# Optimization experiments

Hardware: AMD Instinct MI355X
Metric: run time of the kernel (lower is better)

Reference implementation:

```python
import jax, jax.numpy as jnp
import numpy as np

N = 131072   # number of profile points
S = 64       # n_samples (PSF samples per point)
D = H = W = 256


def setup_inputs() -> dict:
    key = jax.random.key(0)
    k1, k2, k3, k4, k5, k6 = jax.random.split(key, 6)
    x = jax.random.normal(k1, (1, 1, D, H, W), dtype=jnp.float32)
    # voxel-space coordinates (x, y, z) inside the volume
    sampleGrid = jax.random.uniform(k2, (N, 3), dtype=jnp.float32) * jnp.array(
        [W - 1, H - 1, D - 1], dtype=jnp.float32)
    # small axis-angle rotations + translations: [N, 1, 6]
    rot = jax.random.normal(k3, (N, 1, 3), dtype=jnp.float32) * 0.02
    trn = jax.random.normal(k4, (N, 1, 3), dtype=jnp.float32) * 2.0
    ax = jnp.concatenate([rot, trn], axis=-1)
    half = jax.random.uniform(k5, (N, 1, 3), minval=1.0, maxval=3.0, dtype=jnp.float32)
    bound = jnp.concatenate([-half, half], axis=1)  # [N, 2, 3]
    InvCovScaled = jnp.eye(3, dtype=jnp.float32) * 0.5
    # torch.randn(...) - 0.5 from the original forward, hoisted out for determinism
    xyz_psf = jax.random.normal(k6, (N, S, 3), dtype=jnp.float32) - 0.5
    return dict(x=x, sampleGrid=sampleGrid, ax=ax, bound=bound,
                InvCovScaled=InvCovScaled, xyz_psf=xyz_psf)


def _axisangle2mat(a):
    # a: [N, 6] -> [N, 3, 4] = [R | t] via Rodrigues
    v, t = a[:, :3], a[:, 3:]
    theta = jnp.linalg.norm(v, axis=-1, keepdims=True)          # [N,1]
    k = v / jnp.maximum(theta, 1e-12)                            # unit axis
    kx, ky, kz = k[:, 0], k[:, 1], k[:, 2]
    z = jnp.zeros_like(kx)
    K = jnp.stack([z, -kz, ky, kz, z, -kx, -ky, kx, z], axis=-1).reshape(-1, 3, 3)
    ct = jnp.cos(theta)[..., None]  # [N,1,1]
    st = jnp.sin(theta)[..., None]
    I = jnp.eye(3, dtype=a.dtype)
    R = I + st * K + (1.0 - ct) * jnp.matmul(K, K)
    return jnp.concatenate([R, t[..., None]], axis=-1)           # [N,3,4]


def _grid_sample_3d(vol, grid):
    # vol: [D,H,W]; grid: [M,3] normalized coords (x,y,z) in [-1,1]
    # matches F.grid_sample(mode='bilinear', padding_mode='zeros', align_corners=False)
    d, h, w = vol.shape
    sizes = jnp.array([w, h, d], dtype=vol.dtype)
    pix = ((grid + 1.0) * sizes - 1.0) * 0.5                     # unnormalize
    ix, iy, iz = pix[:, 0], pix[:, 1], pix[:, 2]
    x0 = jnp.floor(ix); y0 = jnp.floor(iy); z0 = jnp.floor(iz)
    fx = ix - x0; fy = iy - y0; fz = iz - z0
    x0 = x0.astype(jnp.int32); y0 = y0.astype(jnp.int32); z0 = z0.astype(jnp.int32)

    def gather(xi, yi, zi):
        valid = ((xi >= 0) & (xi < w) & (yi >= 0) & (yi < h) & (zi >= 0) & (zi < d))
        xc = jnp.clip(xi, 0, w - 1)
        yc = jnp.clip(yi, 0, h - 1)
        zc = jnp.clip(zi, 0, d - 1)
        return jnp.where(valid, vol[zc, yc, xc], jnp.zeros((), vol.dtype))

    out = jnp.zeros(grid.shape[0], dtype=vol.dtype)
    for dx in (0, 1):
        wx = fx if dx else (1.0 - fx)
        for dy in (0, 1):
            wy = fy if dy else (1.0 - fy)
            for dz in (0, 1):
                wz = fz if dz else (1.0 - fz)
                out = out + gather(x0 + dx, y0 + dy, z0 + dz) * (wx * wy * wz)
    return out


def reference(x, sampleGrid, ax, bound, InvCovScaled, xyz_psf):
    vol = x[0, 0]                                                # [D,H,W]
    size = jnp.array([x.shape[-1], x.shape[-2], x.shape[-3]], dtype=x.dtype)  # [W,H,D]

    # pose matrices [N,1,3,4]
    mat = _axisangle2mat(ax.reshape(-1, 6)).reshape(ax.shape[:-1] + (3, 4))
    R = mat[..., :3]                                             # [N,1,3,3]
    T = mat[..., 3]                                              # [N,1,3]
    # trans_first=True: p' = R @ (p + T)
    p = sampleGrid[:, None] + T                                  # [N,1,3]
    mat_sampleGrid = jnp.einsum('nkij,nkj->nki', R, p)           # [N,1,3]

    # PSF offsets: [N,S,3]
    bound_psf = xyz_psf * ((bound[:, 1, :] - bound[:, 0, :]) * 0.5)[:, None]
    psf = mat_sampleGrid + bound_psf                             # [N,S,3]

    grid = 2.0 * (psf / (size - 1.0) - 0.5)                      # normalize per-axis
    psf_x = _grid_sample_3d(vol, grid.reshape(-1, 3)).reshape(psf.shape[:-1])  # [N,S]

    center = bound_psf
    q = jnp.einsum('nsi,ij,nsj->ns', center, InvCovScaled, center)
    w = jnp.exp(-0.5 * q)                                        # [N,S]
    y = (psf_x * w).sum(-1) / w.sum(-1)                          # [N]
    return y
```

## Files before the change

kernel.cpp:

```cpp
#include <hip/hip_runtime.h>


#define VOL_N 256
#define S_PSF 64

__global__ __launch_bounds__(256, 4) void psf_sample_kernel(
    const float* __restrict__ vol,
    const float* __restrict__ sampleGrid,
    const float* __restrict__ ax,
    const float* __restrict__ bound,
    const float* __restrict__ invcov,
    const float* __restrict__ xyz_psf,
    float* __restrict__ out,
    int N)
{
    const int lane = threadIdx.x & 63;
    const int n = blockIdx.x * (blockDim.x >> 6) + (threadIdx.x >> 6);
    if (n >= N) return;

    const float vx = ax[n * 6 + 0], vy = ax[n * 6 + 1], vz = ax[n * 6 + 2];
    const float tx = ax[n * 6 + 3], ty = ax[n * 6 + 4], tz = ax[n * 6 + 5];

    const float theta = sqrtf(vx * vx + vy * vy + vz * vz);
    const float kinv = 1.0f / fmaxf(theta, 1e-12f);
    const float kx = vx * kinv, ky = vy * kinv, kz = vz * kinv;
    const float ct = __cosf(theta), st = __sinf(theta);
    const float oc = 1.0f - ct;

    const float r00 = 1.0f + oc * (-(ky * ky + kz * kz));
    const float r01 = -st * kz + oc * kx * ky;
    const float r02 =  st * ky + oc * kx * kz;
    const float r10 =  st * kz + oc * kx * ky;
    const float r11 = 1.0f + oc * (-(kx * kx + kz * kz));
    const float r12 = -st * kx + oc * ky * kz;
    const float r20 = -st * ky + oc * kx * kz;
    const float r21 =  st * kx + oc * ky * kz;
    const float r22 = 1.0f + oc * (-(kx * kx + ky * ky));

    const float px = sampleGrid[n * 3 + 0] + tx;
    const float py = sampleGrid[n * 3 + 1] + ty;
    const float pz = sampleGrid[n * 3 + 2] + tz;

    const float cx = r00 * px + r01 * py + r02 * pz;
    const float cy = r10 * px + r11 * py + r12 * pz;
    const float cz = r20 * px + r21 * py + r22 * pz;

    const float hx = (bound[n * 6 + 3] - bound[n * 6 + 0]) * 0.5f;
    const float hy = (bound[n * 6 + 4] - bound[n * 6 + 1]) * 0.5f;
    const float hz = (bound[n * 6 + 5] - bound[n * 6 + 2]) * 0.5f;

    const float m00 = invcov[0], m01 = invcov[1], m02 = invcov[2];
    const float m10 = invcov[3], m11 = invcov[4], m12 = invcov[5];
    const float m20 = invcov[6], m21 = invcov[7], m22 = invcov[8];

    const long long base = ((long long)n * S_PSF + lane) * 3;
    const float ox = xyz_psf[base + 0] * hx;
    const float oy = xyz_psf[base + 1] * hy;
    const float oz = xyz_psf[base + 2] * hz;

    const float scale = (float)VOL_N / (float)(VOL_N - 1);
    const float ix = (cx + ox) * scale - 0.5f;
    const float iy = (cy + oy) * scale - 0.5f;
    const float iz = (cz + oz) * scale - 0.5f;

    const float x0f = floorf(ix), y0f = floorf(iy), z0f = floorf(iz);
    const float fx = ix - x0f, fy = iy - y0f, fz = iz - z0f;
    const int x0 = (int)x0f, y0 = (int)y0f, z0 = (int)z0f;
    const int x1 = x0 + 1, y1 = y0 + 1, z1 = z0 + 1;

    const bool vx0 = (unsigned)x0 < (unsigned)VOL_N;
    const bool vx1 = (unsigned)x1 < (unsigned)VOL_N;
    const bool vy0 = (unsigned)y0 < (unsigned)VOL_N;
    const bool vy1 = (unsigned)y1 < (unsigned)VOL_N;
    const bool vz0 = (unsigned)z0 < (unsigned)VOL_N;
    const bool vz1 = (unsigned)z1 < (unsigned)VOL_N;

    const int xc0 = min(max(x0, 0), VOL_N - 1);
    const int xc1 = min(max(x1, 0), VOL_N - 1);
    const int yc0 = min(max(y0, 0), VOL_N - 1);
    const int yc1 = min(max(y1, 0), VOL_N - 1);
    const int zc0 = min(max(z0, 0), VOL_N - 1);
    const int zc1 = min(max(z1, 0), VOL_N - 1);

    const int zo0 = zc0 * (VOL_N * VOL_N), zo1 = zc1 * (VOL_N * VOL_N);
    const int yo0 = yc0 * VOL_N, yo1 = yc1 * VOL_N;

    const float v000 = vol[zo0 + yo0 + xc0];
    const float v001 = vol[zo0 + yo0 + xc1];
    const float v010 = vol[zo0 + yo1 + xc0];
    const float v011 = vol[zo0 + yo1 + xc1];
    const float v100 = vol[zo1 + yo0 + xc0];
    const float v101 = vol[zo1 + yo0 + xc1];
    const float v110 = vol[zo1 + yo1 + xc0];
    const float v111 = vol[zo1 + yo1 + xc1];

    const float wx0 = 1.0f - fx, wx1 = fx;
    const float wy0 = 1.0f - fy, wy1 = fy;
    const float wz0 = 1.0f - fz, wz1 = fz;

    float acc = 0.0f;
    acc += (vx0 && vy0 && vz0) ? v000 * (wx0 * wy0 * wz0) : 0.0f;
    acc += (vx1 && vy0 && vz0) ? v001 * (wx1 * wy0 * wz0) : 0.0f;
    acc += (vx0 && vy1 && vz0) ? v010 * (wx0 * wy1 * wz0) : 0.0f;
    acc += (vx1 && vy1 && vz0) ? v011 * (wx1 * wy1 * wz0) : 0.0f;
    acc += (vx0 && vy0 && vz1) ? v100 * (wx0 * wy0 * wz1) : 0.0f;
    acc += (vx1 && vy0 && vz1) ? v101 * (wx1 * wy0 * wz1) : 0.0f;
    acc += (vx0 && vy1 && vz1) ? v110 * (wx0 * wy1 * wz1) : 0.0f;
    acc += (vx1 && vy1 && vz1) ? v111 * (wx1 * wy1 * wz1) : 0.0f;

    const float qx = m00 * ox + m01 * oy + m02 * oz;
    const float qy = m10 * ox + m11 * oy + m12 * oz;
    const float qz = m20 * ox + m21 * oy + m22 * oz;
    const float q = ox * qx + oy * qy + oz * qz;
    const float w = __expf(-0.5f * q);

    float num = acc * w;
    float den = w;
    #pragma unroll
    for (int m = 32; m >= 1; m >>= 1) {
        num += __shfl_xor(num, m, 64);
        den += __shfl_xor(den, m, 64);
    }
    if (lane == 0) out[n] = num / den;
}

extern "C" void kernel_launch(void* const* d_in, const int* in_sizes, int n_in,
                              void* d_out, int out_size, void* d_ws, size_t ws_size,
                              hipStream_t stream) {
    const float* x        = (const float*)d_in[0];
    const float* sg       = (const float*)d_in[1];
    const float* ax       = (const float*)d_in[2];
    const float* bound    = (const float*)d_in[3];
    const float* invcov   = (const float*)d_in[4];
    const float* xyz_psf  = (const float*)d_in[5];
    float* out            = (float*)d_out;

    const int N = in_sizes[1] / 3;
    const int waves_per_block = 4;
    dim3 block(256);
    dim3 grid((N + waves_per_block - 1) / waves_per_block);
    psf_sample_kernel<<<grid, block, 0, stream>>>(x, sg, ax, bound, invcov,
                                                  xyz_psf, out, N);
}
```

Measured before the change: 337.8 us.

## Sort profile points by Morton-ordered spatial bucket to improve volume cache locality

Adds histogram, scan and scatter kernels that bucket the N points by the Morton code of their coarse 16-voxel cell, producing a permutation used by the main kernel. The main kernel also remaps block IDs across the eight XCDs so contiguous sorted chunks share each XCD's L2. The goal is to turn random 64MB volume gathers into spatially coherent accesses with better L2/MALL hit rates. In exchange it adds four small kernel launches, global atomics, and an indirection that makes reads of ax, bound, xyz_psf and out non-coalesced.

```diff
diff --git a/kernel.cpp b/kernel.cpp
--- a/kernel.cpp
+++ b/kernel.cpp
@@ -3,6 +3,61 @@
 
 #define VOL_N 256
 #define S_PSF 64
+#define NBUCKET 4096
+
+
+__device__ __forceinline__ int bucket_of(const float* __restrict__ sg, int n) {
+    int cx = min(max((int)sg[n * 3 + 0], 0), VOL_N - 1) >> 4;
+    int cy = min(max((int)sg[n * 3 + 1], 0), VOL_N - 1) >> 4;
+    int cz = min(max((int)sg[n * 3 + 2], 0), VOL_N - 1) >> 4;
+    int m = 0;
+    #pragma unroll
+    for (int b = 0; b < 4; b++) {
+        m |= (((cx >> b) & 1) << (3 * b))
+           | (((cy >> b) & 1) << (3 * b + 1))
+           | (((cz >> b) & 1) << (3 * b + 2));
+    }
+    return m;
+}
+
+__global__ void zero_hist_kernel(int* __restrict__ ws) {
+    int i = blockIdx.x * blockDim.x + threadIdx.x;
+    if (i < NBUCKET) ws[i] = 0;
+}
+
+__global__ void hist_kernel(const float* __restrict__ sg, int* __restrict__ ws, int N) {
+    int n = blockIdx.x * blockDim.x + threadIdx.x;
+    if (n >= N) return;
+    atomicAdd(&ws[bucket_of(sg, n)], 1);
+}
+
+__global__ __launch_bounds__(1024) void scan_kernel(int* __restrict__ ws) {
+    __shared__ int tmp[1024];
+    const int t = threadIdx.x;
+    int h0 = ws[t * 4 + 0], h1 = ws[t * 4 + 1], h2 = ws[t * 4 + 2], h3 = ws[t * 4 + 3];
+    int s = h0 + h1 + h2 + h3;
+    tmp[t] = s;
+    __syncthreads();
+    for (int off = 1; off < 1024; off <<= 1) {
+        int v = (t >= off) ? tmp[t - off] : 0;
+        __syncthreads();
+        tmp[t] += v;
+        __syncthreads();
+    }
+    int excl = tmp[t] - s;
+    ws[NBUCKET + t * 4 + 0] = excl;
+    ws[NBUCKET + t * 4 + 1] = excl + h0;
+    ws[NBUCKET + t * 4 + 2] = excl + h0 + h1;
+    ws[NBUCKET + t * 4 + 3] = excl + h0 + h1 + h2;
+}
+
+__global__ void scatter_kernel(const float* __restrict__ sg, int* __restrict__ ws, int N) {
+    int n = blockIdx.x * blockDim.x + threadIdx.x;
+    if (n >= N) return;
+    int b = bucket_of(sg, n);
+    int pos = atomicAdd(&ws[NBUCKET + b], 1);
+    ws[2 * NBUCKET + pos] = n;
+}
 
 __global__ __launch_bounds__(256, 4) void psf_sample_kernel(
     const float* __restrict__ vol,
@@ -11,12 +66,19 @@
     const float* __restrict__ bound,
     const float* __restrict__ invcov,
     const float* __restrict__ xyz_psf,
+    const int* __restrict__ perm,
     float* __restrict__ out,
     int N)
 {
     const int lane = threadIdx.x & 63;
-    const int n = blockIdx.x * (blockDim.x >> 6) + (threadIdx.x >> 6);
-    if (n >= N) return;
+
+    int bid = blockIdx.x;
+    const int nb = gridDim.x;
+    if ((nb & 7) == 0) bid = (bid & 7) * (nb >> 3) + (bid >> 3);
+
+    const int i = bid * (blockDim.x >> 6) + (threadIdx.x >> 6);
+    if (i >= N) return;
+    const int n = perm ? perm[i] : i;
 
     const float vx = ax[n * 6 + 0], vy = ax[n * 6 + 1], vz = ax[n * 6 + 2];
     const float tx = ax[n * 6 + 3], ty = ax[n * 6 + 4], tz = ax[n * 6 + 5];
@@ -136,9 +198,21 @@
     float* out            = (float*)d_out;
 
     const int N = in_sizes[1] / 3;
+    const size_t ws_needed = (size_t)(2 * NBUCKET + N) * sizeof(int);
+
+    int* perm = nullptr;
+    if (ws_size >= ws_needed) {
+        int* ws = (int*)d_ws;
+        zero_hist_kernel<<<(NBUCKET + 255) / 256, 256, 0, stream>>>(ws);
+        hist_kernel<<<(N + 255) / 256, 256, 0, stream>>>(sg, ws, N);
+        scan_kernel<<<1, 1024, 0, stream>>>(ws);
+        scatter_kernel<<<(N + 255) / 256, 256, 0, stream>>>(sg, ws, N);
+        perm = ws + 2 * NBUCKET;
+    }
+
     const int waves_per_block = 4;
     dim3 block(256);
     dim3 grid((N + waves_per_block - 1) / waves_per_block);
     psf_sample_kernel<<<grid, block, 0, stream>>>(x, sg, ax, bound, invcov,
-                                                  xyz_psf, out, N);
-}
+                                                  xyz_psf, perm, out, N);
+}
```

Result: faster. 327.9 us (-2.9%).
